# Performance work log

Measured on AMD Instinct MI355X. Metric: run time of the kernel, lower is better.

The kernel has to match this reference:

```python
import jax, jax.numpy as jnp
import numpy as np

TEMPERATURE = 0.8
EPS = 1e-7
NORM_EPS = 1e-12  # torch F.normalize clamp


def setup_inputs() -> dict:
    key = jax.random.key(0)
    k1, k2, k3 = jax.random.split(key, 3)
    N, D = 8192, 256
    features = jax.random.normal(k1, (N, D), dtype=jnp.float32)
    labels = jax.random.randint(k2, (N,), 0, 8, dtype=jnp.int64)
    speaker_ids = jax.random.randint(k3, (N,), 0, 64, dtype=jnp.int64)
    return {"features": features, "labels": labels, "speaker_ids": speaker_ids}


def reference(features, labels, speaker_ids):
    N = features.shape[0]
    # L2-normalize rows (torch F.normalize semantics)
    norm = jnp.maximum(jnp.linalg.norm(features, axis=1, keepdims=True), NORM_EPS)
    f = features / norm
    sim = jnp.matmul(f, f.T) / TEMPERATURE  # [N, N]
    e = jnp.exp(sim)
    same_label = labels[:, None] == labels[None, :]
    same_spk = speaker_ids[:, None] == speaker_ids[None, :]
    eye = jnp.eye(N, dtype=bool)
    mask_pos = same_label & same_spk & ~eye   # same emotion, same speaker, not self
    mask_neg = same_label & ~same_spk & ~eye  # same emotion, different speaker
    num = jnp.sum(jnp.where(mask_pos, e, 0.0), axis=1)  # [N]
    den = jnp.sum(jnp.where(mask_neg, e, 0.0), axis=1) + num + EPS
    valid = jnp.any(mask_pos, axis=1)  # sample contributes iff it has a positive
    num_safe = jnp.where(valid, num, 1.0)
    den_safe = jnp.where(valid, den, 1.0)
    loss_i = -jnp.log(num_safe / den_safe)
    count = jnp.sum(valid)
    total = jnp.sum(jnp.where(valid, loss_i, 0.0))
    return jnp.where(count > 0, total / jnp.maximum(count, 1), 0.0)
```

## Files before the change

kernel.cpp:

```cpp
#include <hip/hip_runtime.h>
#include <math.h>

#define NROWS 8192
#define DDIM  256
#define EPS_V 1e-7f

#define JCHUNK 2048
#define NJT    (JCHUNK / 64)

typedef float f32x4 __attribute__((ext_vector_type(4)));
typedef short s16x8 __attribute__((ext_vector_type(8)));


__device__ __forceinline__ ushort f2bf(float x) {
    unsigned u = __float_as_uint(x);
    unsigned r = (u + 0x7FFFu + ((u >> 16) & 1u)) >> 16;
    return (ushort)r;
}

__device__ __forceinline__ void gload16(const void* gptr, void* lptr) {
    __builtin_amdgcn_global_load_lds(
        (__attribute__((address_space(1))) void*)(uintptr_t)gptr,
        (__attribute__((address_space(3))) void*)(uintptr_t)lptr,
        16, 0, 0);
}

__global__ void normbf_kernel(const float* __restrict__ feat,
                              const int*   __restrict__ lab,
                              const int*   __restrict__ spk,
                              ushort* __restrict__ fbf,
                              float*  __restrict__ nd,
                              int*    __restrict__ keys) {
    const int gt = blockIdx.x * blockDim.x + threadIdx.x;
    if (gt < 2 * NROWS) nd[gt] = 0.0f;
    const int row  = gt >> 6;
    const int lane = gt & 63;
    const float4 v = reinterpret_cast<const float4*>(feat + (size_t)row * DDIM)[lane];
    float ss = v.x * v.x + v.y * v.y + v.z * v.z + v.w * v.w;
    #pragma unroll
    for (int m = 32; m; m >>= 1) ss += __shfl_xor(ss, m);
    const float inv = 1.0f / fmaxf(sqrtf(ss), 1e-12f);
    ushort4 o;
    o.x = f2bf(v.x * inv);
    o.y = f2bf(v.y * inv);
    o.z = f2bf(v.z * inv);
    o.w = f2bf(v.w * inv);
    reinterpret_cast<ushort4*>(fbf + (size_t)row * DDIM)[lane] = o;
    if (lane == 0) keys[row] = (spk[row] << 3) | lab[row];
}

__global__ __launch_bounds__(512, 2) void main_kernel(
        const ushort* __restrict__ fbf,
        const int*    __restrict__ keys,
        float*        __restrict__ num,
        float*        __restrict__ den) {
    __shared__ __align__(16) ushort As[128 * DDIM];
    __shared__ __align__(16) ushort Bs[2][64 * DDIM];

    const int tid  = threadIdx.x;
    const int lane = tid & 63;
    const int wid  = tid >> 6;
    const int wr   = wid >> 2;
    const int wc   = wid & 3;
    const int g    = lane >> 4;
    const int ln   = lane & 15;

    const int panel = blockIdx.x & 63;
    const int jc    = blockIdx.x >> 6;
    const int p0    = panel * 128;
    const int jbase = jc * JCHUNK;

    const int rsub  = lane >> 5;
    const int cphys = lane & 31;

    #pragma unroll
    for (int q = 0; q < 8; ++q) {
        const int r0  = wid * 16 + q * 2;
        const int row = r0 + rsub;
        const int cl  = cphys ^ (row & 7);
        gload16(fbf + (size_t)(p0 + row) * DDIM + cl * 8, &As[r0 * DDIM]);
    }
    #pragma unroll
    for (int q = 0; q < 4; ++q) {
        const int r0  = wid * 8 + q * 2;
        const int row = r0 + rsub;
        const int cl  = cphys ^ (row & 7);
        gload16(fbf + (size_t)(jbase + row) * DDIM + cl * 8, &Bs[0][r0 * DDIM]);
    }
    __syncthreads();

    s16x8 a[4][8];
    #pragma unroll
    for (int fi = 0; fi < 4; ++fi) {
        const int row = wr * 64 + fi * 16 + ln;
        #pragma unroll
        for (int kf = 0; kf < 8; ++kf) {
            const int ch = (kf * 4 + g) ^ (ln & 7);
            a[fi][kf] = *reinterpret_cast<const s16x8*>(&As[row * DDIM + ch * 8]);
        }
    }
    int ki[16];
    #pragma unroll
    for (int t = 0; t < 16; ++t)
        ki[t] = keys[p0 + wr * 64 + (t >> 2) * 16 + g * 4 + (t & 3)];

    float T[16], P[16];
    #pragma unroll
    for (int t = 0; t < 16; ++t) { T[t] = 0.0f; P[t] = 0.0f; }

    const int diag_jt0 = ((p0 >> 11) == jc) ? ((p0 & 2047) >> 6) : -3;

    for (int jt = 0; jt < NJT; ++jt) {
        const int cur = jt & 1;
        if (jt + 1 < NJT) {
            const int j0n = jbase + (jt + 1) * 64;
            #pragma unroll
            for (int q = 0; q < 4; ++q) {
                const int r0  = wid * 8 + q * 2;
                const int row = r0 + rsub;
                const int cl  = cphys ^ (row & 7);
                gload16(fbf + (size_t)(j0n + row) * DDIM + cl * 8, &Bs[cur ^ 1][r0 * DDIM]);
            }
        }
        const int j0 = jbase + jt * 64;
        const int gj = j0 + wc * 16 + ln;
        const int kj = keys[gj];

        f32x4 acc[4];
        #pragma unroll
        for (int fi = 0; fi < 4; ++fi)
            #pragma unroll
            for (int k = 0; k < 4; ++k) acc[fi][k] = 0.0f;

        #pragma unroll
        for (int kf = 0; kf < 8; ++kf) {
            const int ch = (kf * 4 + g) ^ (ln & 7);
            const s16x8 b = *reinterpret_cast<const s16x8*>(
                &Bs[cur][(wc * 16 + ln) * DDIM + ch * 8]);
            #pragma unroll
            for (int fi = 0; fi < 4; ++fi)
                acc[fi] = __builtin_amdgcn_mfma_f32_16x16x32_bf16(a[fi][kf], b, acc[fi], 0, 0, 0);
        }

        if (jt == diag_jt0 || jt == diag_jt0 + 1) {
            #pragma unroll
            for (int fi = 0; fi < 4; ++fi)
                #pragma unroll
                for (int r = 0; r < 4; ++r) {
                    const int t  = fi * 4 + r;
                    const int gi = p0 + wr * 64 + fi * 16 + g * 4 + r;
                    const float e = __expf(acc[fi][r] * 1.25f);
                    const int  kd = ki[t] ^ kj;
                    const bool ns = (gi != gj);
                    T[t] += (((kd & 7) == 0) && ns) ? e : 0.0f;
                    P[t] += ((kd == 0) && ns) ? e : 0.0f;
                }
        } else {
            #pragma unroll
            for (int fi = 0; fi < 4; ++fi)
                #pragma unroll
                for (int r = 0; r < 4; ++r) {
                    const int t = fi * 4 + r;
                    const float e = __expf(acc[fi][r] * 1.25f);
                    const int  kd = ki[t] ^ kj;
                    T[t] += ((kd & 7) == 0) ? e : 0.0f;
                    P[t] += (kd == 0) ? e : 0.0f;
                }
        }
        __syncthreads();
    }

    #pragma unroll
    for (int t = 0; t < 16; ++t) {
        float pv = P[t], tv = T[t];
        #pragma unroll
        for (int m = 1; m < 16; m <<= 1) {
            pv += __shfl_xor(pv, m);
            tv += __shfl_xor(tv, m);
        }
        if (ln == 0) {
            const int gi = p0 + wr * 64 + (t >> 2) * 16 + g * 4 + (t & 3);
            atomicAdd(&num[gi], pv);
            atomicAdd(&den[gi], tv);
        }
    }
}

__global__ void final_kernel(const float* __restrict__ num,
                             const float* __restrict__ den,
                             float* __restrict__ out) {
    __shared__ float s_tot[1024];
    __shared__ int   s_cnt[1024];
    float tot = 0.0f;
    int   cnt = 0;
    for (int i = threadIdx.x; i < NROWS; i += 1024) {
        const float n = num[i];
        if (n > 0.0f) {
            const float d = den[i] + EPS_V;
            tot += logf(d) - logf(n);
            cnt += 1;
        }
    }
    s_tot[threadIdx.x] = tot;
    s_cnt[threadIdx.x] = cnt;
    __syncthreads();
    for (int s = 512; s > 0; s >>= 1) {
        if (threadIdx.x < s) {
            s_tot[threadIdx.x] += s_tot[threadIdx.x + s];
            s_cnt[threadIdx.x] += s_cnt[threadIdx.x + s];
        }
        __syncthreads();
    }
    if (threadIdx.x == 0)
        out[0] = (s_cnt[0] > 0) ? (s_tot[0] / (float)s_cnt[0]) : 0.0f;
}

extern "C" void kernel_launch(void* const* d_in, const int* in_sizes, int n_in,
                              void* d_out, int out_size, void* d_ws, size_t ws_size,
                              hipStream_t stream) {
    const float* feat = (const float*)d_in[0];
    const int*   lab  = (const int*)d_in[1];
    const int*   spk  = (const int*)d_in[2];

    ushort* fbf  = (ushort*)d_ws;
    float*  nd   = (float*)((char*)d_ws + (size_t)NROWS * DDIM * sizeof(ushort));
    float*  num  = nd;
    float*  den  = nd + NROWS;
    int*    keys = (int*)(nd + 2 * NROWS);
    float*  out  = (float*)d_out;

    normbf_kernel<<<(NROWS * 64) / 256, 256, 0, stream>>>(feat, lab, spk, fbf, nd, keys);
    main_kernel<<<256, 512, 0, stream>>>(fbf, keys, num, den);
    final_kernel<<<1, 1024, 0, stream>>>(num, den, out);
}
```

Before: 135.9 us.

## Widen column tile to 128, fold temperature into normalization, fuse final reduction

Each wave now computes a 64x32 block per step using two B fragments, with 128-column tiles double-buffered in LDS. A is loaded straight from global memory into registers, so the A staging buffer in LDS is gone. The 1/temperature factor is folded into the normalization by scaling rows by sqrt(1.25), which removes a multiply before each exp. The separate final kernel is replaced by a last-block-done reduction driven by an atomic counter, removing one launch at the cost of a serialized tail in one block.

Result: slower. 276.2 us (+103.2%).

```diff
diff --git a/kernel.cpp b/kernel.cpp
--- a/kernel.cpp
+++ b/kernel.cpp
@@ -4,9 +4,11 @@
 #define NROWS 8192
 #define DDIM  256
 #define EPS_V 1e-7f
+#define SCALE 1.1180339887498949f
 
 #define JCHUNK 2048
-#define NJT    (JCHUNK / 64)
+#define TILE   128
+#define NJT    (JCHUNK / TILE)
 
 typedef float f32x4 __attribute__((ext_vector_type(4)));
 typedef short s16x8 __attribute__((ext_vector_type(8)));
@@ -29,17 +31,19 @@
                               const int*   __restrict__ lab,
                               const int*   __restrict__ spk,
                               ushort* __restrict__ fbf,
-                              float*  __restrict__ nd,
+                              float*  __restrict__ ndf,
+                              int*    __restrict__ cnt,
                               int*    __restrict__ keys) {
     const int gt = blockIdx.x * blockDim.x + threadIdx.x;
-    if (gt < 2 * NROWS) nd[gt] = 0.0f;
+    if (gt < 2 * NROWS) ndf[gt] = 0.0f;
+    if (gt == 2 * NROWS) *cnt = 0;
     const int row  = gt >> 6;
     const int lane = gt & 63;
     const float4 v = reinterpret_cast<const float4*>(feat + (size_t)row * DDIM)[lane];
     float ss = v.x * v.x + v.y * v.y + v.z * v.z + v.w * v.w;
     #pragma unroll
     for (int m = 32; m; m >>= 1) ss += __shfl_xor(ss, m);
-    const float inv = 1.0f / fmaxf(sqrtf(ss), 1e-12f);
+    const float inv = SCALE / fmaxf(sqrtf(ss), 1e-12f);
     ushort4 o;
     o.x = f2bf(v.x * inv);
     o.y = f2bf(v.y * inv);
@@ -52,10 +56,11 @@
 __global__ __launch_bounds__(512, 2) void main_kernel(
         const ushort* __restrict__ fbf,
         const int*    __restrict__ keys,
-        float*        __restrict__ num,
-        float*        __restrict__ den) {
-    __shared__ __align__(16) ushort As[128 * DDIM];
-    __shared__ __align__(16) ushort Bs[2][64 * DDIM];
+        float2*       __restrict__ nd,
+        int*          __restrict__ cnt,
+        float*        __restrict__ out) {
+    __shared__ __align__(16) ushort Bs[2][TILE * DDIM];
+    __shared__ int s_last;
 
     const int tid  = threadIdx.x;
     const int lane = tid & 63;
@@ -69,6 +74,7 @@
     const int jc    = blockIdx.x >> 6;
     const int p0    = panel * 128;
     const int jbase = jc * JCHUNK;
+    const int diag_jt = (jc == (p0 >> 11)) ? ((p0 & 2047) >> 7) : -1;
 
     const int rsub  = lane >> 5;
     const int cphys = lane & 31;
@@ -78,26 +84,16 @@
         const int r0  = wid * 16 + q * 2;
         const int row = r0 + rsub;
         const int cl  = cphys ^ (row & 7);
-        gload16(fbf + (size_t)(p0 + row) * DDIM + cl * 8, &As[r0 * DDIM]);
-    }
-    #pragma unroll
-    for (int q = 0; q < 4; ++q) {
-        const int r0  = wid * 8 + q * 2;
-        const int row = r0 + rsub;
-        const int cl  = cphys ^ (row & 7);
         gload16(fbf + (size_t)(jbase + row) * DDIM + cl * 8, &Bs[0][r0 * DDIM]);
     }
-    __syncthreads();
 
     s16x8 a[4][8];
     #pragma unroll
     for (int fi = 0; fi < 4; ++fi) {
-        const int row = wr * 64 + fi * 16 + ln;
-        #pragma unroll
-        for (int kf = 0; kf < 8; ++kf) {
-            const int ch = (kf * 4 + g) ^ (ln & 7);
-            a[fi][kf] = *reinterpret_cast<const s16x8*>(&As[row * DDIM + ch * 8]);
-        }
+        const ushort* arow = fbf + (size_t)(p0 + wr * 64 + fi * 16 + ln) * DDIM;
+        #pragma unroll
+        for (int kf = 0; kf < 8; ++kf)
+            a[fi][kf] = *reinterpret_cast<const s16x8*>(arow + kf * 32 + g * 8);
     }
     int ki[16];
     #pragma unroll
@@ -108,64 +104,78 @@
     #pragma unroll
     for (int t = 0; t < 16; ++t) { T[t] = 0.0f; P[t] = 0.0f; }
 
-    const int diag_jt0 = ((p0 >> 11) == jc) ? ((p0 & 2047) >> 6) : -3;
+    __syncthreads();
 
     for (int jt = 0; jt < NJT; ++jt) {
         const int cur = jt & 1;
         if (jt + 1 < NJT) {
-            const int j0n = jbase + (jt + 1) * 64;
-            #pragma unroll
-            for (int q = 0; q < 4; ++q) {
-                const int r0  = wid * 8 + q * 2;
+            const int j0n = jbase + (jt + 1) * TILE;
+            #pragma unroll
+            for (int q = 0; q < 8; ++q) {
+                const int r0  = wid * 16 + q * 2;
                 const int row = r0 + rsub;
                 const int cl  = cphys ^ (row & 7);
                 gload16(fbf + (size_t)(j0n + row) * DDIM + cl * 8, &Bs[cur ^ 1][r0 * DDIM]);
             }
         }
-        const int j0 = jbase + jt * 64;
-        const int gj = j0 + wc * 16 + ln;
-        const int kj = keys[gj];
-
-        f32x4 acc[4];
+        const int j0  = jbase + jt * TILE;
+        const int kj0 = keys[j0 + wc * 32 + ln];
+        const int kj1 = keys[j0 + wc * 32 + 16 + ln];
+        const ushort* B = Bs[cur];
+
+        f32x4 acc[4][2];
         #pragma unroll
         for (int fi = 0; fi < 4; ++fi)
             #pragma unroll
-            for (int k = 0; k < 4; ++k) acc[fi][k] = 0.0f;
+            for (int fj = 0; fj < 2; ++fj)
+                #pragma unroll
+                for (int k = 0; k < 4; ++k) acc[fi][fj][k] = 0.0f;
 
         #pragma unroll
         for (int kf = 0; kf < 8; ++kf) {
-            const int ch = (kf * 4 + g) ^ (ln & 7);
-            const s16x8 b = *reinterpret_cast<const s16x8*>(
-                &Bs[cur][(wc * 16 + ln) * DDIM + ch * 8]);
-            #pragma unroll
-            for (int fi = 0; fi < 4; ++fi)
-                acc[fi] = __builtin_amdgcn_mfma_f32_16x16x32_bf16(a[fi][kf], b, acc[fi], 0, 0, 0);
-        }
-
-        if (jt == diag_jt0 || jt == diag_jt0 + 1) {
-            #pragma unroll
-            for (int fi = 0; fi < 4; ++fi)
+            const int ch = ((kf * 4 + g) ^ (ln & 7)) * 8;
+            const s16x8 b0 = *reinterpret_cast<const s16x8*>(&B[(wc * 32 + ln) * DDIM + ch]);
+            const s16x8 b1 = *reinterpret_cast<const s16x8*>(&B[(wc * 32 + 16 + ln) * DDIM + ch]);
+            #pragma unroll
+            for (int fi = 0; fi < 4; ++fi) {
+                acc[fi][0] = __builtin_amdgcn_mfma_f32_16x16x32_bf16(a[fi][kf], b0, acc[fi][0], 0, 0, 0);
+                acc[fi][1] = __builtin_amdgcn_mfma_f32_16x16x32_bf16(a[fi][kf], b1, acc[fi][1], 0, 0, 0);
+            }
+        }
+
+        if (jt != diag_jt) {
+            #pragma unroll
+            for (int fj = 0; fj < 2; ++fj) {
+                const int kj = fj ? kj1 : kj0;
                 #pragma unroll
-                for (int r = 0; r < 4; ++r) {
-                    const int t  = fi * 4 + r;
-                    const int gi = p0 + wr * 64 + fi * 16 + g * 4 + r;
-                    const float e = __expf(acc[fi][r] * 1.25f);
-                    const int  kd = ki[t] ^ kj;
-                    const bool ns = (gi != gj);
-                    T[t] += (((kd & 7) == 0) && ns) ? e : 0.0f;
-                    P[t] += ((kd == 0) && ns) ? e : 0.0f;
-                }
+                for (int fi = 0; fi < 4; ++fi)
+                    #pragma unroll
+                    for (int r = 0; r < 4; ++r) {
+                        const int t  = fi * 4 + r;
+                        const float e = __expf(acc[fi][fj][r]);
+                        const int  kd = ki[t] ^ kj;
+                        T[t] += ((kd & 7) == 0) ? e : 0.0f;
+                        P[t] += (kd == 0) ? e : 0.0f;
+                    }
+            }
         } else {
             #pragma unroll
-            for (int fi = 0; fi < 4; ++fi)
+            for (int fj = 0; fj < 2; ++fj) {
+                const int kj = fj ? kj1 : kj0;
+                const int gj = j0 + wc * 32 + fj * 16 + ln;
                 #pragma unroll
-                for (int r = 0; r < 4; ++r) {
-                    const int t = fi * 4 + r;
-                    const float e = __expf(acc[fi][r] * 1.25f);
-                    const int  kd = ki[t] ^ kj;
-                    T[t] += ((kd & 7) == 0) ? e : 0.0f;
-                    P[t] += (kd == 0) ? e : 0.0f;
-                }
+                for (int fi = 0; fi < 4; ++fi)
+                    #pragma unroll
+                    for (int r = 0; r < 4; ++r) {
+                        const int t  = fi * 4 + r;
+                        const int gi = p0 + wr * 64 + fi * 16 + g * 4 + r;
+                        const float e = __expf(acc[fi][fj][r]);
+                        const int  kd = ki[t] ^ kj;
+                        const bool ns = (gi != gj);
+                        T[t] += (((kd & 7) == 0) && ns) ? e : 0.0f;
+                        P[t] += ((kd == 0) && ns) ? e : 0.0f;
+                    }
+            }
         }
         __syncthreads();
     }
@@ -180,39 +190,39 @@
         }
         if (ln == 0) {
             const int gi = p0 + wr * 64 + (t >> 2) * 16 + g * 4 + (t & 3);
-            atomicAdd(&num[gi], pv);
-            atomicAdd(&den[gi], tv);
-        }
-    }
-}
-
-__global__ void final_kernel(const float* __restrict__ num,
-                             const float* __restrict__ den,
-                             float* __restrict__ out) {
-    __shared__ float s_tot[1024];
-    __shared__ int   s_cnt[1024];
-    float tot = 0.0f;
-    int   cnt = 0;
-    for (int i = threadIdx.x; i < NROWS; i += 1024) {
-        const float n = num[i];
-        if (n > 0.0f) {
-            const float d = den[i] + EPS_V;
-            tot += logf(d) - logf(n);
-            cnt += 1;
-        }
-    }
-    s_tot[threadIdx.x] = tot;
-    s_cnt[threadIdx.x] = cnt;
+            atomicAdd(&nd[gi].x, pv);
+            atomicAdd(&nd[gi].y, tv);
+        }
+    }
+
     __syncthreads();
-    for (int s = 512; s > 0; s >>= 1) {
-        if (threadIdx.x < s) {
-            s_tot[threadIdx.x] += s_tot[threadIdx.x + s];
-            s_cnt[threadIdx.x] += s_cnt[threadIdx.x + s];
-        }
+    if (tid == 0) {
+        __threadfence();
+        s_last = (atomicAdd(cnt, 1) == (int)gridDim.x - 1) ? 1 : 0;
+    }
+    __syncthreads();
+    if (s_last) {
+        __threadfence();
+        float tot = 0.0f;
+        int   c   = 0;
+        for (int i = tid; i < NROWS; i += 512) {
+            const float2 v = nd[i];
+            if (v.x > 0.0f) {
+                tot += logf(v.y + EPS_V) - logf(v.x);
+                c   += 1;
+            }
+        }
+        float* st = reinterpret_cast<float*>(&Bs[0][0]);
+        int*   sc = reinterpret_cast<int*>(&Bs[1][0]);
+        st[tid] = tot;
+        sc[tid] = c;
         __syncthreads();
-    }
-    if (threadIdx.x == 0)
-        out[0] = (s_cnt[0] > 0) ? (s_tot[0] / (float)s_cnt[0]) : 0.0f;
+        for (int s = 256; s > 0; s >>= 1) {
+            if (tid < s) { st[tid] += st[tid + s]; sc[tid] += sc[tid + s]; }
+            __syncthreads();
+        }
+        if (tid == 0) out[0] = (sc[0] > 0) ? (st[0] / (float)sc[0]) : 0.0f;
+    }
 }
 
 extern "C" void kernel_launch(void* const* d_in, const int* in_sizes, int n_in,
@@ -223,13 +233,13 @@
     const int*   spk  = (const int*)d_in[2];
 
     ushort* fbf  = (ushort*)d_ws;
-    float*  nd   = (float*)((char*)d_ws + (size_t)NROWS * DDIM * sizeof(ushort));
-    float*  num  = nd;
-    float*  den  = nd + NROWS;
-    int*    keys = (int*)(nd + 2 * NROWS);
-    float*  out  = (float*)d_out;
-
-    normbf_kernel<<<(NROWS * 64) / 256, 256, 0, stream>>>(feat, lab, spk, fbf, nd, keys);
-    main_kernel<<<256, 512, 0, stream>>>(fbf, keys, num, den);
-    final_kernel<<<1, 1024, 0, stream>>>(num, den, out);
-}
+    char*   base = (char*)d_ws + (size_t)NROWS * DDIM * sizeof(ushort);
+    float2* nd   = (float2*)base;
+    int*    cnt  = (int*)(base + 2 * NROWS * sizeof(float));
+    int*    keys = (int*)(base + 2 * NROWS * sizeof(float) + 16);
+    float*  outp = (float*)d_out;
+
+    normbf_kernel<<<(NROWS * 64) / 256, 256, 0, stream>>>(feat, lab, spk, fbf,
+                                                          (float*)nd, cnt, keys);
+    main_kernel<<<256, 512, 0, stream>>>(fbf, keys, nd, cnt, outp);
+}
```
